# Performance work log

Measured on AMD Instinct MI355X. Metric: run time of the kernel, lower is better.

Reference implementation:

```python
import jax, jax.numpy as jnp
import numpy as np

E = 8      # num_experts
D = 1024   # input_size
H = 2048   # expert hidden
O = 1024   # output_size
N = 8192   # tokens


def setup_inputs() -> dict:
    key = jax.random.key(0)
    ks = jax.random.split(key, 7)
    s_in = 1.0 / np.sqrt(D)
    s_h = 1.0 / np.sqrt(H)
    return {
        "x": jax.random.normal(ks[0], (N, D), dtype=jnp.float32),
        "Wr": jax.random.normal(ks[1], (D, E), dtype=jnp.float32) * s_in,
        "br": jnp.zeros((E,), dtype=jnp.float32),
        "W1": jax.random.normal(ks[2], (E, D, H), dtype=jnp.float32) * s_in,
        "b1": jnp.zeros((E, H), dtype=jnp.float32),
        "W2": jax.random.normal(ks[3], (E, H, O), dtype=jnp.float32) * s_h,
        "b2": jnp.zeros((E, O), dtype=jnp.float32),
    }


def _moe(x, Wr, br, W1, b1, W2, b2):
    # Supervised top-1 router: softmax probs, argmax route.
    router_probs = jax.nn.softmax(x @ Wr + br, axis=-1)          # [N, E]
    p_max = jnp.max(router_probs, axis=-1)                       # [N]
    routes = jnp.argmax(router_probs, axis=-1)                   # [N] int
    one_hot = jax.nn.one_hot(routes, E, dtype=x.dtype)           # [N, E]
    counts = one_hot.sum(axis=0)                                 # [E]

    # Per-expert 2-layer MLP on all tokens (vectorized over experts),
    # then select the routed expert's output per token. This is the
    # dense-equivalent of the torch gather/per-expert-forward/scatter.
    h = jax.nn.relu(jnp.einsum("nd,edh->enh", x, W1) + b1[:, None, :])   # [E, N, H]
    ys = jnp.einsum("enh,eho->eno", h, W2) + b2[:, None, :]              # [E, N, O]
    out = jnp.einsum("ne,eno->no", one_hot, ys)                          # [N, O]

    # Straight-through scaling: p_max / sg(p_max) == 1 in fwd, routes grad to router.
    ratio = p_max / jax.lax.stop_gradient(p_max)
    out = out * ratio[:, None]
    return out, router_probs, counts


def reference(x, Wr, br, W1, b1, W2, b2):
    return _moe(x, Wr, br, W1, b1, W2, b2)
```

## Files before the change

### kernel.cpp

```cpp
#include <hip/hip_runtime.h>
#include <hip/hip_bf16.h>

#define NTOK 8192
#define DIN  1024
#define HID  2048
#define OUTD 1024
#define NEXP 8
#define BM 128
#define MAXT (NTOK / BM + NEXP)

#define T1BLK 4096
#define RTBLK (NTOK / 4)
#define T2BLK 4096
#define G1BLK ((HID / 128) * MAXT)

typedef short short8 __attribute__((ext_vector_type(8)));
typedef float f32x4 __attribute__((ext_vector_type(4)));

static __device__ __forceinline__ unsigned short f2bf(float f) {
  union { __hip_bfloat16 b; unsigned short u; } cv;
  cv.b = __float2bfloat16(f);
  return cv.u;
}

static __device__ __forceinline__ void gload_lds16(const void* g, void* l) {
  __builtin_amdgcn_global_load_lds(
      (const __attribute__((address_space(1))) void*)g,
      (__attribute__((address_space(3))) void*)l, 16, 0, 0);
}

static __device__ void transpose_body(const float* __restrict__ W,
                                      unsigned short* __restrict__ WT,
                                      int R, int C, int bx, int by, int e,
                                      float* smemf) {
  float (*tile)[65] = (float(*)[65])smemf;
  const int c0 = bx * 64, r0 = by * 64;
  const int lr = threadIdx.x >> 4;
  const int fc = threadIdx.x & 15;
  const float* Wp = W + ((size_t)e * R + r0) * C + c0;
#pragma unroll
  for (int i = 0; i < 4; ++i) {
    int r = lr + i * 16;
    float4 v = *(const float4*)(Wp + (size_t)r * C + fc * 4);
    tile[r][fc * 4 + 0] = v.x; tile[r][fc * 4 + 1] = v.y;
    tile[r][fc * 4 + 2] = v.z; tile[r][fc * 4 + 3] = v.w;
  }
  __syncthreads();
  unsigned short* Op = WT + ((size_t)e * C + c0) * R + r0;
  const int cc0 = threadIdx.x >> 3;
  const int rc = threadIdx.x & 7;
#pragma unroll
  for (int i = 0; i < 2; ++i) {
    int cc = cc0 + i * 32;
    short8 o;
#pragma unroll
    for (int j = 0; j < 8; ++j) o[j] = (short)f2bf(tile[rc * 8 + j][cc]);
    *(short8*)(Op + (size_t)cc * R + rc * 8) = o;
  }
}

static __device__ void router_body(const float* __restrict__ x,
                                   const float* __restrict__ Wr,
                                   const float* __restrict__ br,
                                   unsigned short* __restrict__ xb,
                                   float* __restrict__ probs_out,
                                   int* __restrict__ routes,
                                   int blk, float* smemf) {
  float (*WrL)[DIN] = (float(*)[DIN])smemf;
  const int tid = threadIdx.x;
  {
    const int r0 = tid * 4;
    float wlo[4][4], whi[4][4];
#pragma unroll
    for (int rr = 0; rr < 4; ++rr) {
      float4 v0 = *(const float4*)(Wr + (size_t)(r0 + rr) * NEXP);
      float4 v1 = *(const float4*)(Wr + (size_t)(r0 + rr) * NEXP + 4);
      wlo[rr][0] = v0.x; wlo[rr][1] = v0.y; wlo[rr][2] = v0.z; wlo[rr][3] = v0.w;
      whi[rr][0] = v1.x; whi[rr][1] = v1.y; whi[rr][2] = v1.z; whi[rr][3] = v1.w;
    }
#pragma unroll
    for (int e = 0; e < 4; ++e) {
      float4 o = { wlo[0][e], wlo[1][e], wlo[2][e], wlo[3][e] };
      *(float4*)&WrL[e][r0] = o;
      float4 o2 = { whi[0][e], whi[1][e], whi[2][e], whi[3][e] };
      *(float4*)&WrL[e + 4][r0] = o2;
    }
  }
  __syncthreads();

  const int lane = tid & 63;
  const int n = blk * 4 + (tid >> 6);
  const float4* xr = (const float4*)(x + (size_t)n * DIN);
  ushort4* xo = (ushort4*)(xb + (size_t)n * DIN);
  float acc[NEXP];
#pragma unroll
  for (int e = 0; e < NEXP; ++e) acc[e] = 0.f;
#pragma unroll
  for (int j = 0; j < 4; ++j) {
    int idx = j * 64 + lane;
    float4 xv = xr[idx];
    ushort4 o = { f2bf(xv.x), f2bf(xv.y), f2bf(xv.z), f2bf(xv.w) };
    xo[idx] = o;
    int r0 = idx * 4;
#pragma unroll
    for (int e = 0; e < NEXP; ++e) {
      float4 wv = *(const float4*)&WrL[e][r0];
      acc[e] += xv.x * wv.x + xv.y * wv.y + xv.z * wv.z + xv.w * wv.w;
    }
  }
#pragma unroll
  for (int m = 1; m < 64; m <<= 1)
#pragma unroll
    for (int e = 0; e < NEXP; ++e) acc[e] += __shfl_xor(acc[e], m);

  if (lane == 0) {
    float lg[NEXP], p[NEXP];
    float mx = -1e30f;
#pragma unroll
    for (int e = 0; e < NEXP; ++e) { lg[e] = acc[e] + br[e]; mx = fmaxf(mx, lg[e]); }
    float s = 0.f;
#pragma unroll
    for (int e = 0; e < NEXP; ++e) { p[e] = expf(lg[e] - mx); s += p[e]; }
    float inv = 1.f / s;
    int best = 0; float bp = -1.f;
#pragma unroll
    for (int e = 0; e < NEXP; ++e) {
      p[e] *= inv;
      probs_out[(size_t)n * NEXP + e] = p[e];
      if (p[e] > bp) { bp = p[e]; best = e; }
    }
    routes[n] = best;
  }
}

__global__ __launch_bounds__(256) void prep1_kernel(
    const float* __restrict__ W1, unsigned short* __restrict__ w1t,
    const float* __restrict__ x, const float* __restrict__ Wr,
    const float* __restrict__ br, unsigned short* __restrict__ xb,
    float* __restrict__ probs_out, int* __restrict__ routes) {
  __shared__ float smemf[8192];
  const int bid = blockIdx.x;
  if (bid < T1BLK) {
    int e = bid >> 9, rem = bid & 511;
    transpose_body(W1, w1t, DIN, HID, rem & 31, rem >> 5, e, smemf);
  } else {
    router_body(x, Wr, br, xb, probs_out, routes, bid - T1BLK, smemf);
  }
}

__global__ __launch_bounds__(256) void hist_scan_kernel(
    const int* __restrict__ routes, int* __restrict__ pad_off,
    int2* __restrict__ tile_table, float* __restrict__ counts_out,
    int* __restrict__ cursor, int* __restrict__ sorted) {
  __shared__ int wsum[4][NEXP];
  __shared__ int pstart[NEXP], pend[NEXP];
  const int tid = threadIdx.x;
  const int lane = tid & 63, w = tid >> 6;
  int cnt[NEXP];
#pragma unroll
  for (int e = 0; e < NEXP; ++e) cnt[e] = 0;
#pragma unroll
  for (int j = 0; j < 8; ++j) {
    int4 r4 = ((const int4*)routes)[tid + 256 * j];
    int rr[4] = {r4.x, r4.y, r4.z, r4.w};
#pragma unroll
    for (int i = 0; i < 4; ++i)
#pragma unroll
      for (int e = 0; e < NEXP; ++e) cnt[e] += (rr[i] == e);
  }
#pragma unroll
  for (int m = 1; m < 64; m <<= 1)
#pragma unroll
    for (int e = 0; e < NEXP; ++e) cnt[e] += __shfl_xor(cnt[e], m);
  if (lane == 0)
#pragma unroll
    for (int e = 0; e < NEXP; ++e) wsum[w][e] = cnt[e];
  __syncthreads();
  if (tid == 0) {
    int off = 0, t = 0;
    for (int e = 0; e < NEXP; ++e) {
      int c = wsum[0][e] + wsum[1][e] + wsum[2][e] + wsum[3][e];
      pad_off[e] = off;
      cursor[e] = 0;
      counts_out[e] = (float)c;
      int tiles = (c + BM - 1) / BM;
      pstart[e] = off + c;
      pend[e] = off + tiles * BM;
      for (int i = 0; i < tiles; ++i) { tile_table[t] = make_int2(e, off + i * BM); ++t; }
      off += tiles * BM;
    }
    for (; t < MAXT; ++t) tile_table[t] = make_int2(-1, 0);
  }
  __syncthreads();
#pragma unroll
  for (int e = 0; e < NEXP; ++e)
    for (int i = pstart[e] + tid; i < pend[e]; i += 256) sorted[i] = -1;
}

__global__ void build_kernel(const int* __restrict__ routes,
                             const int* __restrict__ pad_off,
                             int* __restrict__ cursor,
                             int* __restrict__ sorted) {
  const int n = blockIdx.x * 256 + threadIdx.x;
  const int lane = threadIdx.x & 63;
  const int e = routes[n];
#pragma unroll
  for (int ex = 0; ex < NEXP; ++ex) {
    unsigned long long m = __ballot(e == ex);
    if (e == ex) {
      int leader = __ffsll(m) - 1;
      int rank = __popcll(m & ((1ull << lane) - 1ull));
      int b = 0;
      if (rank == 0) b = atomicAdd(&cursor[ex], (int)__popcll(m));
      b = __shfl(b, leader);
      sorted[pad_off[ex] + b + rank] = n;
    }
  }
}

#define PHASE_SYNC() do { \
    __builtin_amdgcn_sched_barrier(0); \
    __builtin_amdgcn_s_barrier(); \
    __builtin_amdgcn_sched_barrier(0); \
    asm volatile("s_waitcnt lgkmcnt(0)" ::: "memory"); \
    __builtin_amdgcn_sched_barrier(0); } while (0)
#define VM4()  asm volatile("s_waitcnt vmcnt(4)" ::: "memory")
#define VM0()  asm volatile("s_waitcnt vmcnt(0)" ::: "memory")

#define LDA(MH, D) \
  _Pragma("unroll") for (int i_ = 0; i_ < 2; ++i_) \
  _Pragma("unroll") for (int k_ = 0; k_ < 2; ++k_) \
    fa[MH][i_][k_] = *(const short8*)&lds[(D) + (MH) * 4096 + aoff[i_][k_]];
#define LDB(NH, D) \
  _Pragma("unroll") for (int j_ = 0; j_ < 2; ++j_) \
  _Pragma("unroll") for (int k_ = 0; k_ < 2; ++k_) \
    fb[j_][k_] = *(const short8*)&lds[(D) + 8192 + (NH) * 4096 + boff[j_][k_]];
#define MFMA_QUAD(MH, NH) do { __builtin_amdgcn_s_setprio(1); \
  _Pragma("unroll") for (int i_ = 0; i_ < 2; ++i_) \
  _Pragma("unroll") for (int j_ = 0; j_ < 2; ++j_) \
  _Pragma("unroll") for (int k_ = 0; k_ < 2; ++k_) \
    acc[(MH) * 2 + i_][(NH) * 2 + j_] = __builtin_amdgcn_mfma_f32_16x16x32_bf16( \
        fa[MH][i_][k_], fb[j_][k_], acc[(MH) * 2 + i_][(NH) * 2 + j_], 0, 0, 0); \
  __builtin_amdgcn_s_setprio(0); } while (0)

template <int KDIM, int MODE, int NB>
static __device__ void gemm_body(
    short* lds, int bid,
    const unsigned short* __restrict__ A, const unsigned short* __restrict__ WT,
    const float* __restrict__ bias, const int* __restrict__ sorted,
    const int2* __restrict__ tile_table, void* __restrict__ Cout, int NDIM) {
  const int nwg = NB * MAXT;
  const int swz = (bid & 7) * (nwg >> 3) + (bid >> 3);
  const int2 tt = tile_table[swz / NB];
  if (tt.x < 0) return;
  const int expert = tt.x, mbase = tt.y;
  const int n0 = (swz % NB) * 128;
  const int tid = threadIdx.x, lane = tid & 63, w = tid >> 6;
  const int qm = w >> 1, qn = w & 1;
  const int fr = lane & 15, klo = lane >> 4;

  const short* srcA[2][2];
  const short* srcB[2][2];
  int dstoff[2];
#pragma unroll
  for (int l = 0; l < 2; ++l) {
    const int ch = l * 256 + tid;
    const int row = ch >> 3;
    const int csw = ((ch & 7) ^ (row & 7)) * 8;
    dstoff[l] = ch * 8;
#pragma unroll
    for (int h = 0; h < 2; ++h) {
      int tok = sorted[mbase + h * 64 + row];
      if (tok < 0) tok = 0;
      srcA[h][l] = (const short*)A + (size_t)tok * KDIM + csw;
      srcB[h][l] = (const short*)WT + ((size_t)expert * NDIM + n0 + h * 64 + row) * KDIM + csw;
    }
  }
  auto stA = [&](int doff, int h, int kt) {
    const int base = doff + h * 4096, ko = kt * 64;
#pragma unroll
    for (int l = 0; l < 2; ++l) gload_lds16(srcA[h][l] + ko, &lds[base + dstoff[l]]);
  };
  auto stB = [&](int doff, int h, int kt) {
    const int base = doff + 8192 + h * 4096, ko = kt * 64;
#pragma unroll
    for (int l = 0; l < 2; ++l) gload_lds16(srcB[h][l] + ko, &lds[base + dstoff[l]]);
  };

  const int rsw = (fr & 7) << 4;
  int aoff[2][2], boff[2][2];
#pragma unroll
  for (int i = 0; i < 2; ++i)
#pragma unroll
    for (int k = 0; k < 2; ++k) {
      int b = (qm * 32 + i * 16 + fr) * 128 + k * 64 + klo * 16;
      aoff[i][k] = (b ^ rsw) >> 1;
    }
#pragma unroll
  for (int j = 0; j < 2; ++j)
#pragma unroll
    for (int k = 0; k < 2; ++k) {
      int b = (qn * 32 + j * 16 + fr) * 128 + k * 64 + klo * 16;
      boff[j][k] = (b ^ rsw) >> 1;
    }

  f32x4 acc[4][4];
#pragma unroll
  for (int mi = 0; mi < 4; ++mi)
#pragma unroll
    for (int nj = 0; nj < 4; ++nj) acc[mi][nj] = (f32x4){0.f, 0.f, 0.f, 0.f};
  short8 fa[2][2][2], fb[2][2];

  constexpr int NKT = KDIM / 64;
  stB(0, 0, 0); stA(0, 1, 0); stB(0, 1, 0); stA(0, 0, 0);
  stB(16384, 0, 1); stA(16384, 1, 1);
  VM4();
  __builtin_amdgcn_s_barrier();
  __builtin_amdgcn_sched_barrier(0);

  for (int t = 0; t < NKT; ++t) {
    const int d = (t & 1) * 16384;
    const int dn = 16384 - d;
    LDA(0, d); LDB(0, d);
    if (t + 1 < NKT) stB(dn, 1, t + 1);
    PHASE_SYNC();
    MFMA_QUAD(0, 0);
    LDA(1, d);
    if (t + 1 < NKT) stA(dn, 0, t + 1);
    PHASE_SYNC();
    MFMA_QUAD(1, 0);
    LDB(1, d);
    if (t + 2 < NKT) stB(d, 0, t + 2);
    PHASE_SYNC();
    MFMA_QUAD(1, 1);
    if (t + 2 < NKT) { stA(d, 1, t + 2); VM4(); } else { VM0(); }
    PHASE_SYNC();
    MFMA_QUAD(0, 1);
  }

  const int fq = lane >> 4;
#pragma unroll
  for (int mi = 0; mi < 4; ++mi) {
    const int rbase = mbase + (mi >> 1) * 64 + qm * 32 + (mi & 1) * 16 + fq * 4;
    int tok[4];
#pragma unroll
    for (int r = 0; r < 4; ++r) tok[r] = sorted[rbase + r];
#pragma unroll
    for (int nj = 0; nj < 4; ++nj) {
      const int col = n0 + (nj >> 1) * 64 + qn * 32 + (nj & 1) * 16 + fr;
      const float bv = bias[(size_t)expert * NDIM + col];
#pragma unroll
      for (int r = 0; r < 4; ++r) {
        if (tok[r] < 0) continue;
        float v = acc[mi][nj][r] + bv;
        if (MODE == 0) {
          ((unsigned short*)Cout)[(size_t)tok[r] * NDIM + col] = f2bf(fmaxf(v, 0.f));
        } else {
          ((float*)Cout)[(size_t)tok[r] * NDIM + col] = v;
        }
      }
    }
  }
}

__global__ __launch_bounds__(256, 2) void gemm1_t2_kernel(
    const unsigned short* __restrict__ xb, const unsigned short* __restrict__ w1t,
    const float* __restrict__ b1, const int* __restrict__ sorted,
    const int2* __restrict__ tile_table, unsigned short* __restrict__ hbuf,
    const float* __restrict__ W2, unsigned short* __restrict__ w2t) {
  __shared__ short lds[32768];
  const int bid = blockIdx.x;
  if (bid < G1BLK) {
    gemm_body<DIN, 0, HID / 128>(lds, bid, xb, w1t, b1, sorted, tile_table,
                                 (void*)hbuf, HID);
  } else {
    int b = bid - G1BLK;
    int e = b >> 9, rem = b & 511;
    transpose_body(W2, w2t, HID, OUTD, rem & 15, rem >> 4, e, (float*)lds);
  }
}

template <int KDIM, int MODE, int NB>
__global__ __launch_bounds__(256, 2) void gemm_moe(
    const unsigned short* __restrict__ A, const unsigned short* __restrict__ WT,
    const float* __restrict__ bias, const int* __restrict__ sorted,
    const int2* __restrict__ tile_table, void* __restrict__ Cout, int NDIM) {
  __shared__ short lds[32768];
  gemm_body<KDIM, MODE, NB>(lds, blockIdx.x, A, WT, bias, sorted, tile_table,
                            Cout, NDIM);
}

extern "C" void kernel_launch(void* const* d_in, const int* in_sizes, int n_in,
                              void* d_out, int out_size, void* d_ws, size_t ws_size,
                              hipStream_t stream) {
  const float* x  = (const float*)d_in[0];
  const float* Wr = (const float*)d_in[1];
  const float* br = (const float*)d_in[2];
  const float* W1 = (const float*)d_in[3];
  const float* b1 = (const float*)d_in[4];
  const float* W2 = (const float*)d_in[5];
  const float* b2 = (const float*)d_in[6];

  float* out_y      = (float*)d_out;
  float* out_probs  = out_y + (size_t)NTOK * OUTD;
  float* out_counts = out_probs + (size_t)NTOK * NEXP;

  char* ws = (char*)d_ws;
  unsigned short* xb   = (unsigned short*)(ws);
  unsigned short* w1t  = (unsigned short*)(ws + 16777216ULL);
  unsigned short* w2t  = (unsigned short*)(ws + 50331648ULL);
  unsigned short* hbuf = (unsigned short*)(ws + 83886080ULL);
  char* p = ws + 117440512ULL;
  int* routes   = (int*)p; p += 32768;
  int* sorted   = (int*)p; p += (NTOK + NEXP * BM) * 4;
  int* cursor   = (int*)p; p += 256;
  int* pad_off  = (int*)p; p += 256;
  int2* tt      = (int2*)p;

  prep1_kernel<<<T1BLK + RTBLK, 256, 0, stream>>>(
      W1, w1t, x, Wr, br, xb, out_probs, routes);
  hist_scan_kernel<<<1, 256, 0, stream>>>(routes, pad_off, tt, out_counts,
                                          cursor, sorted);
  build_kernel<<<NTOK / 256, 256, 0, stream>>>(routes, pad_off, cursor, sorted);
  gemm1_t2_kernel<<<G1BLK + T2BLK, 256, 0, stream>>>(
      xb, w1t, b1, sorted, tt, hbuf, W2, w2t);
  gemm_moe<HID, 1, OUTD / 128><<<(OUTD / 128) * MAXT, 256, 0, stream>>>(
      hbuf, w2t, b2, sorted, tt, out_y, OUTD);
}
```

Baseline: 183.4 us.

## Merge histogram and scatter kernels, replace pipelined GEMM loop with single-buffer loop

Folds the route histogram, prefix scan and token scatter into one single-block kernel that stages routes in shared memory and writes sorted indices deterministically, removing a launch and the atomics. The GEMM main loop drops its hand-tuned double-buffered, phase-interleaved schedule and instead loads one K tile, syncs, then runs all MFMAs. LDS per block is halved and the occupancy hint raised to 3 blocks per CU, trading software pipelining for more resident waves. The serial 32-element-per-thread scatter and the loss of load/compute overlap inside each block may cost latency.

New measurement: 171.1 us. -6.7%, faster.

```diff
diff --git a/kernel.cpp b/kernel.cpp
--- a/kernel.cpp
+++ b/kernel.cpp
@@ -148,40 +148,42 @@
   }
 }
 
-__global__ __launch_bounds__(256) void hist_scan_kernel(
+__global__ __launch_bounds__(256) void hist_build_kernel(
     const int* __restrict__ routes, int* __restrict__ pad_off,
     int2* __restrict__ tile_table, float* __restrict__ counts_out,
-    int* __restrict__ cursor, int* __restrict__ sorted) {
-  __shared__ int wsum[4][NEXP];
-  __shared__ int pstart[NEXP], pend[NEXP];
+    int* __restrict__ sorted) {
+  __shared__ int rloc[NTOK];
+  __shared__ int cpre[256][NEXP];
+  __shared__ int tot[NEXP], pstart[NEXP], pend[NEXP];
   const int tid = threadIdx.x;
-  const int lane = tid & 63, w = tid >> 6;
+#pragma unroll
+  for (int j = 0; j < 8; ++j)
+    ((int4*)rloc)[tid + 256 * j] = ((const int4*)routes)[tid + 256 * j];
+  __syncthreads();
+
+  const int t0 = tid * 32;
   int cnt[NEXP];
 #pragma unroll
   for (int e = 0; e < NEXP; ++e) cnt[e] = 0;
-#pragma unroll
-  for (int j = 0; j < 8; ++j) {
-    int4 r4 = ((const int4*)routes)[tid + 256 * j];
-    int rr[4] = {r4.x, r4.y, r4.z, r4.w};
-#pragma unroll
-    for (int i = 0; i < 4; ++i)
-#pragma unroll
-      for (int e = 0; e < NEXP; ++e) cnt[e] += (rr[i] == e);
-  }
-#pragma unroll
-  for (int m = 1; m < 64; m <<= 1)
-#pragma unroll
-    for (int e = 0; e < NEXP; ++e) cnt[e] += __shfl_xor(cnt[e], m);
-  if (lane == 0)
-#pragma unroll
-    for (int e = 0; e < NEXP; ++e) wsum[w][e] = cnt[e];
+  for (int i = 0; i < 32; ++i) {
+    int r = rloc[t0 + i];
+#pragma unroll
+    for (int e = 0; e < NEXP; ++e) cnt[e] += (r == e);
+  }
+#pragma unroll
+  for (int e = 0; e < NEXP; ++e) cpre[tid][e] = cnt[e];
+  __syncthreads();
+  if (tid < NEXP) {
+    int run = 0;
+    for (int i = 0; i < 256; ++i) { int c = cpre[i][tid]; cpre[i][tid] = run; run += c; }
+    tot[tid] = run;
+  }
   __syncthreads();
   if (tid == 0) {
     int off = 0, t = 0;
     for (int e = 0; e < NEXP; ++e) {
-      int c = wsum[0][e] + wsum[1][e] + wsum[2][e] + wsum[3][e];
+      int c = tot[e];
       pad_off[e] = off;
-      cursor[e] = 0;
       counts_out[e] = (float)c;
       int tiles = (c + BM - 1) / BM;
       pstart[e] = off + c;
@@ -192,56 +194,19 @@
     for (; t < MAXT; ++t) tile_table[t] = make_int2(-1, 0);
   }
   __syncthreads();
+  int pos[NEXP];
+#pragma unroll
+  for (int e = 0; e < NEXP; ++e) pos[e] = pad_off[e] + cpre[tid][e];
+  for (int i = 0; i < 32; ++i) {
+    int r = rloc[t0 + i];
+#pragma unroll
+    for (int e = 0; e < NEXP; ++e)
+      if (r == e) { sorted[pos[e]] = t0 + i; ++pos[e]; }
+  }
 #pragma unroll
   for (int e = 0; e < NEXP; ++e)
     for (int i = pstart[e] + tid; i < pend[e]; i += 256) sorted[i] = -1;
 }
-
-__global__ void build_kernel(const int* __restrict__ routes,
-                             const int* __restrict__ pad_off,
-                             int* __restrict__ cursor,
-                             int* __restrict__ sorted) {
-  const int n = blockIdx.x * 256 + threadIdx.x;
-  const int lane = threadIdx.x & 63;
-  const int e = routes[n];
-#pragma unroll
-  for (int ex = 0; ex < NEXP; ++ex) {
-    unsigned long long m = __ballot(e == ex);
-    if (e == ex) {
-      int leader = __ffsll(m) - 1;
-      int rank = __popcll(m & ((1ull << lane) - 1ull));
-      int b = 0;
-      if (rank == 0) b = atomicAdd(&cursor[ex], (int)__popcll(m));
-      b = __shfl(b, leader);
-      sorted[pad_off[ex] + b + rank] = n;
-    }
-  }
-}
-
-#define PHASE_SYNC() do { \
-    __builtin_amdgcn_sched_barrier(0); \
-    __builtin_amdgcn_s_barrier(); \
-    __builtin_amdgcn_sched_barrier(0); \
-    asm volatile("s_waitcnt lgkmcnt(0)" ::: "memory"); \
-    __builtin_amdgcn_sched_barrier(0); } while (0)
-#define VM4()  asm volatile("s_waitcnt vmcnt(4)" ::: "memory")
-#define VM0()  asm volatile("s_waitcnt vmcnt(0)" ::: "memory")
-
-#define LDA(MH, D) \
-  _Pragma("unroll") for (int i_ = 0; i_ < 2; ++i_) \
-  _Pragma("unroll") for (int k_ = 0; k_ < 2; ++k_) \
-    fa[MH][i_][k_] = *(const short8*)&lds[(D) + (MH) * 4096 + aoff[i_][k_]];
-#define LDB(NH, D) \
-  _Pragma("unroll") for (int j_ = 0; j_ < 2; ++j_) \
-  _Pragma("unroll") for (int k_ = 0; k_ < 2; ++k_) \
-    fb[j_][k_] = *(const short8*)&lds[(D) + 8192 + (NH) * 4096 + boff[j_][k_]];
-#define MFMA_QUAD(MH, NH) do { __builtin_amdgcn_s_setprio(1); \
-  _Pragma("unroll") for (int i_ = 0; i_ < 2; ++i_) \
-  _Pragma("unroll") for (int j_ = 0; j_ < 2; ++j_) \
-  _Pragma("unroll") for (int k_ = 0; k_ < 2; ++k_) \
-    acc[(MH) * 2 + i_][(NH) * 2 + j_] = __builtin_amdgcn_mfma_f32_16x16x32_bf16( \
-        fa[MH][i_][k_], fb[j_][k_], acc[(MH) * 2 + i_][(NH) * 2 + j_], 0, 0, 0); \
-  __builtin_amdgcn_s_setprio(0); } while (0)
 
 template <int KDIM, int MODE, int NB>
 static __device__ void gemm_body(
@@ -259,49 +224,32 @@
   const int qm = w >> 1, qn = w & 1;
   const int fr = lane & 15, klo = lane >> 4;
 
-  const short* srcA[2][2];
-  const short* srcB[2][2];
-  int dstoff[2];
-#pragma unroll
-  for (int l = 0; l < 2; ++l) {
-    const int ch = l * 256 + tid;
+  const short* srcA[4];
+  const short* srcB[4];
+  int dstA[4], dstB[4];
+#pragma unroll
+  for (int i = 0; i < 4; ++i) {
+    const int ch = i * 256 + tid;
     const int row = ch >> 3;
     const int csw = ((ch & 7) ^ (row & 7)) * 8;
-    dstoff[l] = ch * 8;
-#pragma unroll
-    for (int h = 0; h < 2; ++h) {
-      int tok = sorted[mbase + h * 64 + row];
-      if (tok < 0) tok = 0;
-      srcA[h][l] = (const short*)A + (size_t)tok * KDIM + csw;
-      srcB[h][l] = (const short*)WT + ((size_t)expert * NDIM + n0 + h * 64 + row) * KDIM + csw;
-    }
-  }
-  auto stA = [&](int doff, int h, int kt) {
-    const int base = doff + h * 4096, ko = kt * 64;
-#pragma unroll
-    for (int l = 0; l < 2; ++l) gload_lds16(srcA[h][l] + ko, &lds[base + dstoff[l]]);
-  };
-  auto stB = [&](int doff, int h, int kt) {
-    const int base = doff + 8192 + h * 4096, ko = kt * 64;
-#pragma unroll
-    for (int l = 0; l < 2; ++l) gload_lds16(srcB[h][l] + ko, &lds[base + dstoff[l]]);
-  };
+    int tok = sorted[mbase + row];
+    if (tok < 0) tok = 0;
+    srcA[i] = (const short*)A + (size_t)tok * KDIM + csw;
+    srcB[i] = (const short*)WT + ((size_t)expert * NDIM + n0 + row) * KDIM + csw;
+    dstA[i] = ch * 8;
+    dstB[i] = 8192 + ch * 8;
+  }
 
   const int rsw = (fr & 7) << 4;
-  int aoff[2][2], boff[2][2];
-#pragma unroll
-  for (int i = 0; i < 2; ++i)
+  int aoff[4][2], boff[4][2];
+#pragma unroll
+  for (int i = 0; i < 4; ++i)
 #pragma unroll
     for (int k = 0; k < 2; ++k) {
-      int b = (qm * 32 + i * 16 + fr) * 128 + k * 64 + klo * 16;
-      aoff[i][k] = (b ^ rsw) >> 1;
-    }
-#pragma unroll
-  for (int j = 0; j < 2; ++j)
-#pragma unroll
-    for (int k = 0; k < 2; ++k) {
-      int b = (qn * 32 + j * 16 + fr) * 128 + k * 64 + klo * 16;
-      boff[j][k] = (b ^ rsw) >> 1;
+      int ba = (qm * 64 + i * 16 + fr) * 128 + k * 64 + klo * 16;
+      aoff[i][k] = (ba ^ rsw) >> 1;
+      int bb = (qn * 64 + i * 16 + fr) * 128 + k * 64 + klo * 16;
+      boff[i][k] = ((bb ^ rsw) >> 1) + 8192;
     }
 
   f32x4 acc[4][4];
@@ -309,45 +257,47 @@
   for (int mi = 0; mi < 4; ++mi)
 #pragma unroll
     for (int nj = 0; nj < 4; ++nj) acc[mi][nj] = (f32x4){0.f, 0.f, 0.f, 0.f};
-  short8 fa[2][2][2], fb[2][2];
 
   constexpr int NKT = KDIM / 64;
-  stB(0, 0, 0); stA(0, 1, 0); stB(0, 1, 0); stA(0, 0, 0);
-  stB(16384, 0, 1); stA(16384, 1, 1);
-  VM4();
-  __builtin_amdgcn_s_barrier();
-  __builtin_amdgcn_sched_barrier(0);
-
   for (int t = 0; t < NKT; ++t) {
-    const int d = (t & 1) * 16384;
-    const int dn = 16384 - d;
-    LDA(0, d); LDB(0, d);
-    if (t + 1 < NKT) stB(dn, 1, t + 1);
-    PHASE_SYNC();
-    MFMA_QUAD(0, 0);
-    LDA(1, d);
-    if (t + 1 < NKT) stA(dn, 0, t + 1);
-    PHASE_SYNC();
-    MFMA_QUAD(1, 0);
-    LDB(1, d);
-    if (t + 2 < NKT) stB(d, 0, t + 2);
-    PHASE_SYNC();
-    MFMA_QUAD(1, 1);
-    if (t + 2 < NKT) { stA(d, 1, t + 2); VM4(); } else { VM0(); }
-    PHASE_SYNC();
-    MFMA_QUAD(0, 1);
+    if (t) __syncthreads();
+    const int ko = t * 64;
+#pragma unroll
+    for (int i = 0; i < 4; ++i) {
+      gload_lds16(srcA[i] + ko, &lds[dstA[i]]);
+      gload_lds16(srcB[i] + ko, &lds[dstB[i]]);
+    }
+    __syncthreads();
+    short8 a[4][2], b[4][2];
+#pragma unroll
+    for (int i = 0; i < 4; ++i)
+#pragma unroll
+      for (int k = 0; k < 2; ++k) {
+        a[i][k] = *(const short8*)&lds[aoff[i][k]];
+        b[i][k] = *(const short8*)&lds[boff[i][k]];
+      }
+    __builtin_amdgcn_s_setprio(1);
+#pragma unroll
+    for (int mi = 0; mi < 4; ++mi)
+#pragma unroll
+      for (int nj = 0; nj < 4; ++nj)
+#pragma unroll
+        for (int k = 0; k < 2; ++k)
+          acc[mi][nj] = __builtin_amdgcn_mfma_f32_16x16x32_bf16(
+              a[mi][k], b[nj][k], acc[mi][nj], 0, 0, 0);
+    __builtin_amdgcn_s_setprio(0);
   }
 
   const int fq = lane >> 4;
 #pragma unroll
   for (int mi = 0; mi < 4; ++mi) {
-    const int rbase = mbase + (mi >> 1) * 64 + qm * 32 + (mi & 1) * 16 + fq * 4;
+    const int rbase = mbase + qm * 64 + mi * 16 + fq * 4;
     int tok[4];
 #pragma unroll
     for (int r = 0; r < 4; ++r) tok[r] = sorted[rbase + r];
 #pragma unroll
     for (int nj = 0; nj < 4; ++nj) {
-      const int col = n0 + (nj >> 1) * 64 + qn * 32 + (nj & 1) * 16 + fr;
+      const int col = n0 + qn * 64 + nj * 16 + fr;
       const float bv = bias[(size_t)expert * NDIM + col];
 #pragma unroll
       for (int r = 0; r < 4; ++r) {
@@ -363,12 +313,12 @@
   }
 }
 
-__global__ __launch_bounds__(256, 2) void gemm1_t2_kernel(
+__global__ __launch_bounds__(256, 3) void gemm1_t2_kernel(
     const unsigned short* __restrict__ xb, const unsigned short* __restrict__ w1t,
     const float* __restrict__ b1, const int* __restrict__ sorted,
     const int2* __restrict__ tile_table, unsigned short* __restrict__ hbuf,
     const float* __restrict__ W2, unsigned short* __restrict__ w2t) {
-  __shared__ short lds[32768];
+  __shared__ short lds[16384];
   const int bid = blockIdx.x;
   if (bid < G1BLK) {
     gemm_body<DIN, 0, HID / 128>(lds, bid, xb, w1t, b1, sorted, tile_table,
@@ -381,11 +331,11 @@
 }
 
 template <int KDIM, int MODE, int NB>
-__global__ __launch_bounds__(256, 2) void gemm_moe(
+__global__ __launch_bounds__(256, 3) void gemm_moe(
     const unsigned short* __restrict__ A, const unsigned short* __restrict__ WT,
     const float* __restrict__ bias, const int* __restrict__ sorted,
     const int2* __restrict__ tile_table, void* __restrict__ Cout, int NDIM) {
-  __shared__ short lds[32768];
+  __shared__ short lds[16384];
   gemm_body<KDIM, MODE, NB>(lds, blockIdx.x, A, WT, bias, sorted, tile_table,
                             Cout, NDIM);
 }
@@ -413,15 +363,13 @@
   char* p = ws + 117440512ULL;
   int* routes   = (int*)p; p += 32768;
   int* sorted   = (int*)p; p += (NTOK + NEXP * BM) * 4;
-  int* cursor   = (int*)p; p += 256;
   int* pad_off  = (int*)p; p += 256;
   int2* tt      = (int2*)p;
 
   prep1_kernel<<<T1BLK + RTBLK, 256, 0, stream>>>(
       W1, w1t, x, Wr, br, xb, out_probs, routes);
-  hist_scan_kernel<<<1, 256, 0, stream>>>(routes, pad_off, tt, out_counts,
-                                          cursor, sorted);
-  build_kernel<<<NTOK / 256, 256, 0, stream>>>(routes, pad_off, cursor, sorted);
+  hist_build_kernel<<<1, 256, 0, stream>>>(routes, pad_off, tt, out_counts,
+                                           sorted);
   gemm1_t2_kernel<<<G1BLK + T2BLK, 256, 0, stream>>>(
       xb, w1t, b1, sorted, tt, hbuf, W2, w2t);
   gemm_moe<HID, 1, OUTD / 128><<<(OUTD / 128) * MAXT, 256, 0, stream>>>(
```
